# Performance work log

Hardware: AMD Instinct MI355X
Metric: run time of the kernel (lower is better)

Reference implementation:

```python
import jax, jax.numpy as jnp
import numpy as np

D_MODEL = 512
D_FF = 2048
VOCAB = 32000
B, N = 2, 384
EPS = 1e-6


def positional_encoding(n, d):
    pos = np.arange(n)[:, None].astype(np.float64)
    i = np.arange(d)[None, :]
    ang = pos / np.power(10000.0, (2 * (i // 2)) / np.float32(d))
    ang[:, 0::2] = np.sin(ang[:, 0::2])
    ang[:, 1::2] = np.cos(ang[:, 1::2])
    return jnp.asarray(ang, dtype=jnp.float32)  # [n, d]


def layer_norm(x, gamma, beta):
    mu = jnp.mean(x, axis=-1, keepdims=True)
    var = jnp.mean(jnp.square(x - mu), axis=-1, keepdims=True)
    return (x - mu) / jnp.sqrt(var + EPS) * gamma + beta


def setup_inputs() -> dict:
    key = jax.random.key(0)
    ks = jax.random.split(key, 12)
    s = 0.02
    return {
        "tokens": jax.random.randint(ks[0], (B, N), 0, VOCAB, dtype=jnp.int32),
        "emb": jax.random.normal(ks[1], (VOCAB, D_MODEL), jnp.float32) * s,
        "Wq": jax.random.normal(ks[2], (D_MODEL, D_MODEL), jnp.float32) * s,
        "bq": jnp.zeros((D_MODEL,), jnp.float32),
        "Wk": jax.random.normal(ks[3], (D_MODEL, D_MODEL), jnp.float32) * s,
        "bk": jnp.zeros((D_MODEL,), jnp.float32),
        "Wv": jax.random.normal(ks[4], (D_MODEL, D_MODEL), jnp.float32) * s,
        "bv": jnp.zeros((D_MODEL,), jnp.float32),
        "attn_scale": jax.random.normal(ks[5], (D_MODEL,), jnp.float32) * 0.05,
        "Wo": jax.random.normal(ks[6], (D_MODEL, D_MODEL), jnp.float32) * s,
        "bo": jnp.zeros((D_MODEL,), jnp.float32),
        "g1": jnp.ones((D_MODEL,), jnp.float32),
        "beta1": jnp.zeros((D_MODEL,), jnp.float32),
        "W1": jax.random.normal(ks[7], (D_MODEL, D_FF), jnp.float32) * s,
        "bf1": jnp.zeros((D_FF,), jnp.float32),
        "W2": jax.random.normal(ks[8], (D_FF, D_MODEL), jnp.float32) * s,
        "bf2": jnp.zeros((D_MODEL,), jnp.float32),
        "g2": jnp.ones((D_MODEL,), jnp.float32),
        "beta2": jnp.zeros((D_MODEL,), jnp.float32),
    }


def reference(tokens, emb, Wq, bq, Wk, bk, Wv, bv, attn_scale, Wo, bo,
              g1, beta1, W1, bf1, W2, bf2, g2, beta2):
    # Embedding + scaled positional encoding
    x = emb[tokens] * jnp.sqrt(jnp.float32(D_MODEL))  # [B, N, D]
    x = x + positional_encoding(N, D_MODEL)[None, :, :]

    # Additive (Bahdanau) self-attention
    q = x @ Wq + bq
    k = x @ Wk + bk  # note: original swaps key/value Dense layers; math-equivalent
    v = x @ Wv + bv
    # scores[b,i,j] = sum_d scale[d] * tanh(q[b,i,d] + k[b,j,d])  -> [B,N,N]
    scores = jnp.einsum("d,bijd->bij", attn_scale,
                        jnp.tanh(q[:, :, None, :] + k[:, None, :, :]))
    weights = jax.nn.softmax(scores, axis=-1)
    attn = jnp.einsum("bij,bjd->bid", weights, v)
    attn = attn @ Wo + bo
    x = layer_norm(x + attn, g1, beta1)

    # Feedforward + residual + LayerNorm
    h = jax.nn.relu(x @ W1 + bf1)
    y = h @ W2 + bf2
    return layer_norm(x + y, g2, beta2)
```

## Files before the change

kernel.cpp:

```cpp
#include <hip/hip_runtime.h>
#include <hip/hip_bf16.h>
#include <math.h>

#define D_MODEL 512
#define D_FF    2048
#define NBATCH  2
#define NSEQ    384
#define NROWS   (NBATCH * NSEQ)
#define LN_EPS  1e-6f

typedef __attribute__((ext_vector_type(8))) short short8;
typedef __attribute__((ext_vector_type(4))) short short4v;
typedef __attribute__((ext_vector_type(4))) float f32x4;
typedef __hip_bfloat16 bf16;

static __device__ __forceinline__ short bfb(float x) {
    bf16 h = __float2bfloat16(x);
    return *reinterpret_cast<short*>(&h);
}

#define MFMA16(a, b, c) __builtin_amdgcn_mfma_f32_16x16x32_bf16((a), (b), (c), 0, 0, 0)

__global__ __launch_bounds__(256) void prep_kernel(
    const int* __restrict__ tokens, const float* __restrict__ emb,
    const float* __restrict__ Wq, const float* __restrict__ Wk,
    const float* __restrict__ Wv, const float* __restrict__ Wo,
    const float* __restrict__ W1, const float* __restrict__ W2,
    bf16* __restrict__ wqt, bf16* __restrict__ wkt, bf16* __restrict__ wvt,
    bf16* __restrict__ wot, bf16* __restrict__ w1t, bf16* __restrict__ w2t,
    float* __restrict__ x, bf16* __restrict__ xb)
{
    __shared__ float tile[32][33];
    int t = blockIdx.x;

    if (t < 3072) {
        const float* W; bf16* Wt; int K, N, bx, by;
        if (t < 1024) {
            int w = t >> 8, rem = t & 255;
            W  = (w == 0) ? Wq  : (w == 1) ? Wk  : (w == 2) ? Wv  : Wo;
            Wt = (w == 0) ? wqt : (w == 1) ? wkt : (w == 2) ? wvt : wot;
            K = 512; N = 512; bx = rem & 15; by = rem >> 4;
        } else if (t < 2048) {
            int rem = t - 1024;
            W = W1; Wt = w1t; K = 512; N = 2048; bx = rem & 63; by = rem >> 6;
        } else {
            int rem = t - 2048;
            W = W2; Wt = w2t; K = 2048; N = 512; bx = rem & 15; by = rem >> 4;
        }
        int tx = threadIdx.x & 31, ty = threadIdx.x >> 5;
        #pragma unroll
        for (int r = ty; r < 32; r += 8)
            tile[r][tx] = W[(size_t)(by * 32 + r) * N + bx * 32 + tx];
        __syncthreads();
        #pragma unroll
        for (int r = ty; r < 32; r += 8)
            Wt[(size_t)(bx * 32 + r) * K + by * 32 + tx] = __float2bfloat16(tile[tx][r]);
    } else {
        int row = t - 3072;
        int n   = row % NSEQ;
        int tok = tokens[row];
        const float sqrtD = 22.627416997969522f;
        const float ESC   = 0.02595256324130752f;
        for (int d = threadIdx.x; d < D_MODEL; d += 256) {
            float e   = emb[tok * D_MODEL + d] * sqrtD;
            float ang = (float)n * __builtin_amdgcn_exp2f(-(float)(d & ~1) * ESC);
            float pe  = (d & 1) ? __cosf(ang) : __sinf(ang);
            float val = e + pe;
            x [(size_t)row * D_MODEL + d] = val;
            xb[(size_t)row * D_MODEL + d] = __float2bfloat16(val);
        }
    }
}

__global__ __launch_bounds__(256) void qkv_mfma_kernel(
    const bf16* __restrict__ A,
    const bf16* __restrict__ wqt, const bf16* __restrict__ wkt, const bf16* __restrict__ wvt,
    const float* __restrict__ bq, const float* __restrict__ bk, const float* __restrict__ bv,
    float* __restrict__ aexp, float* __restrict__ bexp, bf16* __restrict__ vT)
{
    int z = blockIdx.z;
    const bf16*  Wt   = (z == 0) ? wqt : (z == 1) ? wkt : wvt;
    const float* bias = (z == 0) ? bq  : (z == 1) ? bk  : bv;

    int lane = threadIdx.x & 63, wid = threadIdx.x >> 6;
    int rowBase = blockIdx.y * 32 + (wid >> 1) * 16;
    int colBase = blockIdx.x * 64 + (wid & 1) * 32;

    const bf16* Ap  = A  + (size_t)(rowBase + (lane & 15)) * D_MODEL + ((lane >> 4) << 3);
    const bf16* Bp0 = Wt + (size_t)(colBase + (lane & 15)) * D_MODEL + ((lane >> 4) << 3);
    const bf16* Bp1 = Bp0 + (size_t)16 * D_MODEL;

    f32x4 acc0 = {0.f, 0.f, 0.f, 0.f};
    f32x4 acc1 = {0.f, 0.f, 0.f, 0.f};

    #pragma unroll 4
    for (int k0 = 0; k0 < D_MODEL; k0 += 32) {
        short8 a  = *reinterpret_cast<const short8*>(Ap  + k0);
        short8 b0 = *reinterpret_cast<const short8*>(Bp0 + k0);
        short8 b1 = *reinterpret_cast<const short8*>(Bp1 + k0);
        acc0 = MFMA16(a, b0, acc0);
        acc1 = MFMA16(a, b1, acc1);
    }

    int crow = rowBase + ((lane >> 4) << 2);
    int ccol = colBase + (lane & 15);

    if (z < 2) {
        float* C = (z == 0) ? aexp : bexp;
        #pragma unroll
        for (int r = 0; r < 4; ++r) {
            int row = crow + r;
            #pragma unroll
            for (int j = 0; j < 2; ++j) {
                int col = ccol + j * 16;
                float val = (j == 0 ? acc0[r] : acc1[r]) + bias[col];
                C[(size_t)row * D_MODEL + col] = __expf(2.0f * val);
            }
        }
    } else {
        int bb = crow / NSEQ;
        int jr = crow - bb * NSEQ;
        #pragma unroll
        for (int j = 0; j < 2; ++j) {
            int col = ccol + j * 16;
            short4v pk;
            #pragma unroll
            for (int r = 0; r < 4; ++r)
                pk[r] = bfb((j == 0 ? acc0[r] : acc1[r]) + bias[col]);
            size_t idx = ((size_t)bb * D_MODEL + col) * NSEQ + jr;
            *reinterpret_cast<short4v*>((short*)vT + idx) = pk;
        }
    }
}

__global__ __launch_bounds__(512) void score_kernel(
    const float* __restrict__ aexp, const float* __restrict__ bexp,
    const float* __restrict__ scale, bf16* __restrict__ E,
    float* __restrict__ Sp)
{
    int ig   = blockIdx.x;
    int qt   = blockIdx.y;
    int row0 = ig * 4;
    int b    = row0 / NSEQ;
    int tid  = threadIdx.x;
    int lane = tid & 63, wid = tid >> 6;

    __shared__ float sred[8][4];

    const float* ap = aexp + (size_t)row0 * D_MODEL + lane * 8;
    float a[4][8];
    #pragma unroll
    for (int r = 0; r < 4; ++r) {
        float4 A0 = *(const float4*)(ap + (size_t)r * D_MODEL);
        float4 A1 = *(const float4*)(ap + (size_t)r * D_MODEL + 4);
        a[r][0]=A0.x; a[r][1]=A0.y; a[r][2]=A0.z; a[r][3]=A0.w;
        a[r][4]=A1.x; a[r][5]=A1.y; a[r][6]=A1.z; a[r][7]=A1.w;
    }
    float4 S0 = *(const float4*)(scale + lane * 8);
    float4 S1 = *(const float4*)(scale + lane * 8 + 4);
    float sv[8] = {-2.0f*S0.x,-2.0f*S0.y,-2.0f*S0.z,-2.0f*S0.w,
                   -2.0f*S1.x,-2.0f*S1.y,-2.0f*S1.z,-2.0f*S1.w};

    const float* kb = bexp + (size_t)b * NSEQ * D_MODEL + lane * 8;
    int jb = qt * 96 + wid;

    float es[4] = {0.f, 0.f, 0.f, 0.f};

    for (int t6 = 0; t6 < 6; ++t6) {
        int j0 = jb + t6 * 16;
        int j1 = j0 + 8;
        const float4* kp0 = (const float4*)(kb + (size_t)j0 * D_MODEL);
        const float4* kp1 = (const float4*)(kb + (size_t)j1 * D_MODEL);
        float4 xa = kp0[0], xc = kp0[1];
        float4 ya = kp1[0], yc = kp1[1];
        float b0[8] = {xa.x,xa.y,xa.z,xa.w,xc.x,xc.y,xc.z,xc.w};
        float b1[8] = {ya.x,ya.y,ya.z,ya.w,yc.x,yc.y,yc.z,yc.w};

        float u[4][2] = {};
        #pragma unroll
        for (int up = 0; up < 4; ++up) {
            int d0 = up * 2, d1 = d0 + 1;
            #pragma unroll
            for (int js = 0; js < 2; ++js) {
                float xx = js ? b1[d0] : b0[d0];
                float yy = js ? b1[d1] : b0[d1];
                #pragma unroll
                for (int r = 0; r < 4; ++r) {
                    float p   = fmaf(a[r][d0], xx, 1.0f);
                    float q   = fmaf(a[r][d1], yy, 1.0f);
                    float num = fmaf(sv[d0], q, sv[d1] * p);
                    u[r][js]  = fmaf(num, __builtin_amdgcn_rcpf(p * q), u[r][js]);
                }
            }
        }

        #pragma unroll
        for (int off = 1; off < 64; off <<= 1) {
            #pragma unroll
            for (int r = 0; r < 4; ++r) {
                u[r][0] += __shfl_xor(u[r][0], off, 64);
                u[r][1] += __shfl_xor(u[r][1], off, 64);
            }
        }

        #pragma unroll
        for (int r = 0; r < 4; ++r) {
            float e0 = __expf(u[r][0]);
            float e1 = __expf(u[r][1]);
            if (lane == 0) {
                E[(size_t)(row0 + r) * NSEQ + j0] = __float2bfloat16(e0);
                E[(size_t)(row0 + r) * NSEQ + j1] = __float2bfloat16(e1);
            }
            es[r] += e0 + e1;
        }
    }

    if (lane == 0) {
        sred[wid][0] = es[0]; sred[wid][1] = es[1];
        sred[wid][2] = es[2]; sred[wid][3] = es[3];
    }
    __syncthreads();
    if (tid < 4) {
        float s = 0.0f;
        #pragma unroll
        for (int w = 0; w < 8; ++w) s += sred[w][tid];
        Sp[(size_t)(row0 + tid) * 4 + qt] = s;
    }
}

__global__ __launch_bounds__(512) void pv_wo_ln_kernel(
    const bf16* __restrict__ E, const bf16* __restrict__ vT,
    const float* __restrict__ Sp, const bf16* __restrict__ wot,
    const float* __restrict__ bo, const float* __restrict__ x0,
    const float* __restrict__ g1, const float* __restrict__ beta1,
    float* __restrict__ x1, bf16* __restrict__ x1b)
{
    int row0 = blockIdx.x * 16;
    int b    = row0 / NSEQ;
    int tid  = threadIdx.x;
    int lane = tid & 63, wid = tid >> 6;
    int colBase = wid * 64;

    __shared__ bf16  attnS[16][D_MODEL + 8];
    __shared__ float t1f  [16][D_MODEL + 4];

    int arow = lane & 15;
    int koff = (lane >> 4) << 3;
    int crow = (lane >> 4) << 2;
    int ccol = lane & 15;

    {
        const bf16* Ap = E + ((size_t)(row0 + arow)) * NSEQ + koff;
        const bf16* Bp = vT + ((size_t)b * D_MODEL + colBase + arow) * NSEQ + koff;
        f32x4 p0 = {0,0,0,0}, p1 = {0,0,0,0}, p2 = {0,0,0,0}, p3 = {0,0,0,0};
        #pragma unroll
        for (int k0 = 0; k0 < NSEQ; k0 += 32) {
            short8 a  = *(const short8*)(Ap + k0);
            short8 v0 = *(const short8*)(Bp + k0);
            short8 v1 = *(const short8*)(Bp + (size_t)16 * NSEQ + k0);
            short8 v2 = *(const short8*)(Bp + (size_t)32 * NSEQ + k0);
            short8 v3 = *(const short8*)(Bp + (size_t)48 * NSEQ + k0);
            p0 = MFMA16(a, v0, p0);
            p1 = MFMA16(a, v1, p1);
            p2 = MFMA16(a, v2, p2);
            p3 = MFMA16(a, v3, p3);
        }
        #pragma unroll
        for (int r = 0; r < 4; ++r) {
            int lrow = crow + r;
            float4 sp4 = *(const float4*)(Sp + (size_t)(row0 + lrow) * 4);
            float Sinv = 1.0f / (sp4.x + sp4.y + sp4.z + sp4.w);
            attnS[lrow][colBase +  0 + ccol] = __float2bfloat16(p0[r] * Sinv);
            attnS[lrow][colBase + 16 + ccol] = __float2bfloat16(p1[r] * Sinv);
            attnS[lrow][colBase + 32 + ccol] = __float2bfloat16(p2[r] * Sinv);
            attnS[lrow][colBase + 48 + ccol] = __float2bfloat16(p3[r] * Sinv);
        }
    }
    __syncthreads();

    {
        const bf16* Wp = wot + ((size_t)(colBase + arow)) * D_MODEL + koff;
        f32x4 w0 = {0,0,0,0}, w1 = {0,0,0,0}, w2 = {0,0,0,0}, w3 = {0,0,0,0};
        #pragma unroll
        for (int k0 = 0; k0 < D_MODEL; k0 += 32) {
            short8 a  = *(const short8*)(&attnS[arow][k0 + koff]);
            short8 q0 = *(const short8*)(Wp + k0);
            short8 q1 = *(const short8*)(Wp + (size_t)16 * D_MODEL + k0);
            short8 q2 = *(const short8*)(Wp + (size_t)32 * D_MODEL + k0);
            short8 q3 = *(const short8*)(Wp + (size_t)48 * D_MODEL + k0);
            w0 = MFMA16(a, q0, w0);
            w1 = MFMA16(a, q1, w1);
            w2 = MFMA16(a, q2, w2);
            w3 = MFMA16(a, q3, w3);
        }
        #pragma unroll
        for (int r = 0; r < 4; ++r) {
            int lrow = crow + r;
            size_t grow = (size_t)(row0 + lrow);
            int c0 = colBase + ccol;
            t1f[lrow][c0     ] = w0[r] + bo[c0     ] + x0[grow * D_MODEL + c0     ];
            t1f[lrow][c0 + 16] = w1[r] + bo[c0 + 16] + x0[grow * D_MODEL + c0 + 16];
            t1f[lrow][c0 + 32] = w2[r] + bo[c0 + 32] + x0[grow * D_MODEL + c0 + 32];
            t1f[lrow][c0 + 48] = w3[r] + bo[c0 + 48] + x0[grow * D_MODEL + c0 + 48];
        }
    }
    __syncthreads();

    #pragma unroll
    for (int rr = 0; rr < 2; ++rr) {
        int lrow = wid * 2 + rr;
        size_t grow = (size_t)(row0 + lrow);
        float v[8];
        #pragma unroll
        for (int u = 0; u < 8; ++u) v[u] = t1f[lrow][lane * 8 + u];
        float s = 0.0f;
        #pragma unroll
        for (int u = 0; u < 8; ++u) s += v[u];
        #pragma unroll
        for (int off = 1; off < 64; off <<= 1) s += __shfl_xor(s, off, 64);
        float mu = s * (1.0f / D_MODEL);
        float s2 = 0.0f;
        #pragma unroll
        for (int u = 0; u < 8; ++u) { float d = v[u] - mu; s2 += d * d; }
        #pragma unroll
        for (int off = 1; off < 64; off <<= 1) s2 += __shfl_xor(s2, off, 64);
        float inv = rsqrtf(s2 * (1.0f / D_MODEL) + LN_EPS);
        #pragma unroll
        for (int u = 0; u < 8; ++u) {
            int c = lane * 8 + u;
            float o = (v[u] - mu) * inv * g1[c] + beta1[c];
            x1 [grow * D_MODEL + c] = o;
            x1b[grow * D_MODEL + c] = __float2bfloat16(o);
        }
    }
}

__global__ __launch_bounds__(256) void mfma_gemm_kernel(
    const bf16* __restrict__ A, const bf16* __restrict__ Wt,
    const float* __restrict__ bias,
    bf16* __restrict__ Cb, int K, int N, int relu)
{
    int lane = threadIdx.x & 63, wid = threadIdx.x >> 6;
    int rowBase = blockIdx.y * 32 + (wid >> 1) * 16;
    int colBase = blockIdx.x * 64 + (wid & 1) * 32;

    const bf16* Ap  = A  + (size_t)(rowBase + (lane & 15)) * K + ((lane >> 4) << 3);
    const bf16* Bp0 = Wt + (size_t)(colBase + (lane & 15)) * K + ((lane >> 4) << 3);
    const bf16* Bp1 = Bp0 + (size_t)16 * K;

    f32x4 acc0 = {0.f, 0.f, 0.f, 0.f};
    f32x4 acc1 = {0.f, 0.f, 0.f, 0.f};

    #pragma unroll 4
    for (int k0 = 0; k0 < K; k0 += 32) {
        short8 a  = *reinterpret_cast<const short8*>(Ap  + k0);
        short8 b0 = *reinterpret_cast<const short8*>(Bp0 + k0);
        short8 b1 = *reinterpret_cast<const short8*>(Bp1 + k0);
        acc0 = MFMA16(a, b0, acc0);
        acc1 = MFMA16(a, b1, acc1);
    }

    int crow = rowBase + ((lane >> 4) << 2);
    int ccol = colBase + (lane & 15);
    #pragma unroll
    for (int r = 0; r < 4; ++r) {
        int row = crow + r;
        #pragma unroll
        for (int j = 0; j < 2; ++j) {
            int col = ccol + j * 16;
            float val = (j == 0 ? acc0[r] : acc1[r]) + bias[col];
            if (relu) val = fmaxf(val, 0.0f);
            Cb[(size_t)row * N + col] = __float2bfloat16(val);
        }
    }
}

__global__ __launch_bounds__(256) void ffdown_kernel(
    const bf16* __restrict__ A, const bf16* __restrict__ Wt,
    const float* __restrict__ bias, const float* __restrict__ resid,
    float* __restrict__ y0, float* __restrict__ y1)
{
    int z = blockIdx.z;
    int kbeg = z * (D_FF / 2);
    int lane = threadIdx.x & 63, wid = threadIdx.x >> 6;
    int rowBase = blockIdx.y * 32 + (wid >> 1) * 16;
    int colBase = blockIdx.x * 64 + (wid & 1) * 32;

    const bf16* Ap  = A  + (size_t)(rowBase + (lane & 15)) * D_FF + kbeg + ((lane >> 4) << 3);
    const bf16* Bp0 = Wt + (size_t)(colBase + (lane & 15)) * D_FF + kbeg + ((lane >> 4) << 3);
    const bf16* Bp1 = Bp0 + (size_t)16 * D_FF;

    f32x4 acc0 = {0.f, 0.f, 0.f, 0.f};
    f32x4 acc1 = {0.f, 0.f, 0.f, 0.f};

    #pragma unroll 4
    for (int k0 = 0; k0 < D_FF / 2; k0 += 32) {
        short8 a  = *reinterpret_cast<const short8*>(Ap  + k0);
        short8 b0 = *reinterpret_cast<const short8*>(Bp0 + k0);
        short8 b1 = *reinterpret_cast<const short8*>(Bp1 + k0);
        acc0 = MFMA16(a, b0, acc0);
        acc1 = MFMA16(a, b1, acc1);
    }

    int crow = rowBase + ((lane >> 4) << 2);
    int ccol = colBase + (lane & 15);
    #pragma unroll
    for (int r = 0; r < 4; ++r) {
        int row = crow + r;
        #pragma unroll
        for (int j = 0; j < 2; ++j) {
            int col = ccol + j * 16;
            float val = (j == 0 ? acc0[r] : acc1[r]);
            if (z == 0) {
                val += bias[col] + resid[(size_t)row * D_MODEL + col];
                y0[(size_t)row * D_MODEL + col] = val;
            } else {
                y1[(size_t)row * D_MODEL + col] = val;
            }
        }
    }
}

__global__ __launch_bounds__(256) void ln_kernel(
    const float* __restrict__ in, const float* __restrict__ in2,
    const float* __restrict__ gamma, const float* __restrict__ beta,
    float* __restrict__ out)
{
    int row = blockIdx.x;
    int tid = threadIdx.x;
    int lane = tid & 63, wid = tid >> 6;
    __shared__ float red[4];

    float v0 = in[(size_t)row * D_MODEL + tid];
    float v1 = in[(size_t)row * D_MODEL + tid + 256];
    if (in2) {
        v0 += in2[(size_t)row * D_MODEL + tid];
        v1 += in2[(size_t)row * D_MODEL + tid + 256];
    }

    float s = v0 + v1;
    #pragma unroll
    for (int off = 32; off; off >>= 1) s += __shfl_xor(s, off, 64);
    if (lane == 0) red[wid] = s;
    __syncthreads();
    if (tid == 0) red[0] = red[0] + red[1] + red[2] + red[3];
    __syncthreads();
    float mu = red[0] * (1.0f / D_MODEL);
    __syncthreads();

    float d0 = v0 - mu, d1 = v1 - mu;
    float s2 = d0 * d0 + d1 * d1;
    #pragma unroll
    for (int off = 32; off; off >>= 1) s2 += __shfl_xor(s2, off, 64);
    if (lane == 0) red[wid] = s2;
    __syncthreads();
    if (tid == 0) red[0] = red[0] + red[1] + red[2] + red[3];
    __syncthreads();
    float var = red[0] * (1.0f / D_MODEL);
    float inv = rsqrtf(var + LN_EPS);

    out[(size_t)row * D_MODEL + tid]       = d0 * inv * gamma[tid] + beta[tid];
    out[(size_t)row * D_MODEL + tid + 256] = d1 * inv * gamma[tid + 256] + beta[tid + 256];
}

extern "C" void kernel_launch(void* const* d_in, const int* in_sizes, int n_in,
                              void* d_out, int out_size, void* d_ws, size_t ws_size,
                              hipStream_t stream)
{
    const int*   tokens = (const int*)  d_in[0];
    const float* emb    = (const float*)d_in[1];
    const float* Wq     = (const float*)d_in[2];
    const float* bq     = (const float*)d_in[3];
    const float* Wk     = (const float*)d_in[4];
    const float* bk     = (const float*)d_in[5];
    const float* Wv     = (const float*)d_in[6];
    const float* bv     = (const float*)d_in[7];
    const float* ascale = (const float*)d_in[8];
    const float* Wo     = (const float*)d_in[9];
    const float* bo     = (const float*)d_in[10];
    const float* g1     = (const float*)d_in[11];
    const float* beta1  = (const float*)d_in[12];
    const float* W1     = (const float*)d_in[13];
    const float* bf1    = (const float*)d_in[14];
    const float* W2     = (const float*)d_in[15];
    const float* bf2    = (const float*)d_in[16];
    const float* g2     = (const float*)d_in[17];
    const float* beta2  = (const float*)d_in[18];

    float* out = (float*)d_out;
    float* ws  = (float*)d_ws;

    const size_t SZ = (size_t)NROWS * D_MODEL;

    float* x0   = ws;
    float* aexp = ws + 1 * SZ;
    float* bexp = ws + 2 * SZ;
    float* x1 = aexp;
    float* y0 = x1;
    float* y1 = bexp;

    bf16* x0b   = (bf16*)(ws + 3 * SZ);
    bf16* x1b   = x0b + SZ;
    bf16* hb    = x1b + SZ;
    bf16* Eb    = hb + (size_t)NROWS * D_FF;
    bf16* vTb   = Eb + (size_t)NBATCH * NSEQ * NSEQ;
    bf16* wqt   = vTb + (size_t)NBATCH * D_MODEL * NSEQ;
    bf16* wkt   = wqt + (size_t)D_MODEL * D_MODEL;
    bf16* wvt   = wkt + (size_t)D_MODEL * D_MODEL;
    bf16* wot   = wvt + (size_t)D_MODEL * D_MODEL;
    bf16* w1t   = wot + (size_t)D_MODEL * D_MODEL;
    bf16* w2t   = w1t + (size_t)D_MODEL * D_FF;
    float* Sp   = (float*)(w2t + (size_t)D_FF * D_MODEL);

    prep_kernel<<<3072 + NROWS, 256, 0, stream>>>(
        tokens, emb, Wq, Wk, Wv, Wo, W1, W2,
        wqt, wkt, wvt, wot, w1t, w2t, x0, x0b);

    qkv_mfma_kernel<<<dim3(D_MODEL / 64, NROWS / 32, 3), 256, 0, stream>>>(
        x0b, wqt, wkt, wvt, bq, bk, bv, aexp, bexp, vTb);

    score_kernel<<<dim3(NROWS / 4, 4), 512, 0, stream>>>(aexp, bexp, ascale, Eb, Sp);

    pv_wo_ln_kernel<<<NROWS / 16, 512, 0, stream>>>(
        Eb, vTb, Sp, wot, bo, x0, g1, beta1, x1, x1b);

    mfma_gemm_kernel<<<dim3(D_FF / 64, NROWS / 32), 256, 0, stream>>>(
        x1b, w1t, bf1, hb, D_MODEL, D_FF, 1);

    ffdown_kernel<<<dim3(D_MODEL / 64, NROWS / 32, 2), 256, 0, stream>>>(
        hb, w2t, bf2, x1, y0, y1);

    ln_kernel<<<NROWS, 256, 0, stream>>>(y0, y1, g2, beta2, out);
}
```

Baseline: 134.2 us.

## Fuse PV product into score kernel and split Wo projection from LayerNorm

New measurement: 130.5 us. -2.7%, faster.

```diff
diff --git a/kernel.cpp b/kernel.cpp
--- a/kernel.cpp
+++ b/kernel.cpp
@@ -76,7 +76,7 @@
     const bf16* __restrict__ A,
     const bf16* __restrict__ wqt, const bf16* __restrict__ wkt, const bf16* __restrict__ wvt,
     const float* __restrict__ bq, const float* __restrict__ bk, const float* __restrict__ bv,
-    float* __restrict__ aexp, float* __restrict__ bexp, bf16* __restrict__ vT)
+    float* __restrict__ aexp, float* __restrict__ bexp, bf16* __restrict__ vb)
 {
     int z = blockIdx.z;
     const bf16*  Wt   = (z == 0) ? wqt : (z == 1) ? wkt : wvt;
@@ -118,25 +118,23 @@
             }
         }
     } else {
-        int bb = crow / NSEQ;
-        int jr = crow - bb * NSEQ;
-        #pragma unroll
-        for (int j = 0; j < 2; ++j) {
-            int col = ccol + j * 16;
-            short4v pk;
+        #pragma unroll
+        for (int r = 0; r < 4; ++r) {
+            int row = crow + r;
             #pragma unroll
-            for (int r = 0; r < 4; ++r)
-                pk[r] = bfb((j == 0 ? acc0[r] : acc1[r]) + bias[col]);
-            size_t idx = ((size_t)bb * D_MODEL + col) * NSEQ + jr;
-            *reinterpret_cast<short4v*>((short*)vT + idx) = pk;
-        }
-    }
-}
-
-__global__ __launch_bounds__(512) void score_kernel(
+            for (int j = 0; j < 2; ++j) {
+                int col = ccol + j * 16;
+                float val = (j == 0 ? acc0[r] : acc1[r]) + bias[col];
+                vb[(size_t)row * D_MODEL + col] = __float2bfloat16(val);
+            }
+        }
+    }
+}
+
+__global__ __launch_bounds__(512) void scorepv_kernel(
     const float* __restrict__ aexp, const float* __restrict__ bexp,
-    const float* __restrict__ scale, bf16* __restrict__ E,
-    float* __restrict__ Sp)
+    const float* __restrict__ scale, const bf16* __restrict__ vb,
+    float* __restrict__ attn_q, float* __restrict__ Sp)
 {
     int ig   = blockIdx.x;
     int qt   = blockIdx.y;
@@ -145,6 +143,7 @@
     int tid  = threadIdx.x;
     int lane = tid & 63, wid = tid >> 6;
 
+    __shared__ float Et[4][96];
     __shared__ float sred[8][4];
 
     const float* ap = aexp + (size_t)row0 * D_MODEL + lane * 8;
@@ -167,7 +166,9 @@
     float es[4] = {0.f, 0.f, 0.f, 0.f};
 
     for (int t6 = 0; t6 < 6; ++t6) {
-        int j0 = jb + t6 * 16;
+        int jl0 = wid + t6 * 16;
+        int jl1 = jl0 + 8;
+        int j0 = qt * 96 + jl0;
         int j1 = j0 + 8;
         const float4* kp0 = (const float4*)(kb + (size_t)j0 * D_MODEL);
         const float4* kp1 = (const float4*)(kb + (size_t)j1 * D_MODEL);
@@ -207,10 +208,7 @@
         for (int r = 0; r < 4; ++r) {
             float e0 = __expf(u[r][0]);
             float e1 = __expf(u[r][1]);
-            if (lane == 0) {
-                E[(size_t)(row0 + r) * NSEQ + j0] = __float2bfloat16(e0);
-                E[(size_t)(row0 + r) * NSEQ + j1] = __float2bfloat16(e1);
-            }
+            if (lane == 0) { Et[r][jl0] = e0; Et[r][jl1] = e1; }
             es[r] += e0 + e1;
         }
     }
@@ -226,111 +224,93 @@
         for (int w = 0; w < 8; ++w) s += sred[w][tid];
         Sp[(size_t)(row0 + tid) * 4 + qt] = s;
     }
-}
-
-__global__ __launch_bounds__(512) void pv_wo_ln_kernel(
-    const bf16* __restrict__ E, const bf16* __restrict__ vT,
-    const float* __restrict__ Sp, const bf16* __restrict__ wot,
-    const float* __restrict__ bo, const float* __restrict__ x0,
-    const float* __restrict__ g1, const float* __restrict__ beta1,
-    float* __restrict__ x1, bf16* __restrict__ x1b)
-{
-    int row0 = blockIdx.x * 16;
-    int b    = row0 / NSEQ;
-    int tid  = threadIdx.x;
+
+    int d = wid * 64 + lane;
+    const bf16* vcol = vb + ((size_t)b * NSEQ + qt * 96) * D_MODEL + d;
+    float pacc[4] = {0.f, 0.f, 0.f, 0.f};
+    #pragma unroll 4
+    for (int j = 0; j < 96; ++j) {
+        float vf = __bfloat162float(vcol[(size_t)j * D_MODEL]);
+        pacc[0] = fmaf(Et[0][j], vf, pacc[0]);
+        pacc[1] = fmaf(Et[1][j], vf, pacc[1]);
+        pacc[2] = fmaf(Et[2][j], vf, pacc[2]);
+        pacc[3] = fmaf(Et[3][j], vf, pacc[3]);
+    }
+    size_t qbase = (size_t)qt * NROWS * D_MODEL;
+    #pragma unroll
+    for (int r = 0; r < 4; ++r)
+        attn_q[qbase + (size_t)(row0 + r) * D_MODEL + d] = pacc[r];
+}
+
+__global__ __launch_bounds__(256) void wo_kernel(
+    const float* __restrict__ attn_q, const float* __restrict__ Sp,
+    const bf16* __restrict__ wot, const float* __restrict__ bo,
+    const float* __restrict__ x0, float* __restrict__ t1)
+{
+    int rowBase = blockIdx.y * 32;
+    int colBase = blockIdx.x * 64;
+    int tid = threadIdx.x;
+
+    __shared__ bf16  attnS[32][D_MODEL + 8];
+    __shared__ float sinvS[32];
+
+    if (tid < 32) {
+        float4 s4 = *(const float4*)(Sp + (size_t)(rowBase + tid) * 4);
+        sinvS[tid] = 1.0f / (s4.x + s4.y + s4.z + s4.w);
+    }
+    __syncthreads();
+
+    const size_t Q = (size_t)NROWS * D_MODEL;
+    #pragma unroll
+    for (int i = tid; i < 32 * D_MODEL / 4; i += 256) {
+        int r  = i >> 7;
+        int d4 = (i & 127) << 2;
+        size_t off = (size_t)(rowBase + r) * D_MODEL + d4;
+        float4 v0 = *(const float4*)(attn_q + off);
+        float4 v1 = *(const float4*)(attn_q + Q + off);
+        float4 v2 = *(const float4*)(attn_q + 2 * Q + off);
+        float4 v3 = *(const float4*)(attn_q + 3 * Q + off);
+        float si = sinvS[r];
+        short4v pk;
+        pk[0] = bfb((v0.x + v1.x + v2.x + v3.x) * si);
+        pk[1] = bfb((v0.y + v1.y + v2.y + v3.y) * si);
+        pk[2] = bfb((v0.z + v1.z + v2.z + v3.z) * si);
+        pk[3] = bfb((v0.w + v1.w + v2.w + v3.w) * si);
+        *reinterpret_cast<short4v*>(&attnS[r][d4]) = pk;
+    }
+    __syncthreads();
+
     int lane = tid & 63, wid = tid >> 6;
-    int colBase = wid * 64;
-
-    __shared__ bf16  attnS[16][D_MODEL + 8];
-    __shared__ float t1f  [16][D_MODEL + 4];
-
-    int arow = lane & 15;
-    int koff = (lane >> 4) << 3;
-    int crow = (lane >> 4) << 2;
-    int ccol = lane & 15;
-
-    {
-        const bf16* Ap = E + ((size_t)(row0 + arow)) * NSEQ + koff;
-        const bf16* Bp = vT + ((size_t)b * D_MODEL + colBase + arow) * NSEQ + koff;
-        f32x4 p0 = {0,0,0,0}, p1 = {0,0,0,0}, p2 = {0,0,0,0}, p3 = {0,0,0,0};
-        #pragma unroll
-        for (int k0 = 0; k0 < NSEQ; k0 += 32) {
-            short8 a  = *(const short8*)(Ap + k0);
-            short8 v0 = *(const short8*)(Bp + k0);
-            short8 v1 = *(const short8*)(Bp + (size_t)16 * NSEQ + k0);
-            short8 v2 = *(const short8*)(Bp + (size_t)32 * NSEQ + k0);
-            short8 v3 = *(const short8*)(Bp + (size_t)48 * NSEQ + k0);
-            p0 = MFMA16(a, v0, p0);
-            p1 = MFMA16(a, v1, p1);
-            p2 = MFMA16(a, v2, p2);
-            p3 = MFMA16(a, v3, p3);
-        }
-        #pragma unroll
-        for (int r = 0; r < 4; ++r) {
-            int lrow = crow + r;
-            float4 sp4 = *(const float4*)(Sp + (size_t)(row0 + lrow) * 4);
-            float Sinv = 1.0f / (sp4.x + sp4.y + sp4.z + sp4.w);
-            attnS[lrow][colBase +  0 + ccol] = __float2bfloat16(p0[r] * Sinv);
-            attnS[lrow][colBase + 16 + ccol] = __float2bfloat16(p1[r] * Sinv);
-            attnS[lrow][colBase + 32 + ccol] = __float2bfloat16(p2[r] * Sinv);
-            attnS[lrow][colBase + 48 + ccol] = __float2bfloat16(p3[r] * Sinv);
-        }
-    }
-    __syncthreads();
-
-    {
-        const bf16* Wp = wot + ((size_t)(colBase + arow)) * D_MODEL + koff;
-        f32x4 w0 = {0,0,0,0}, w1 = {0,0,0,0}, w2 = {0,0,0,0}, w3 = {0,0,0,0};
-        #pragma unroll
-        for (int k0 = 0; k0 < D_MODEL; k0 += 32) {
-            short8 a  = *(const short8*)(&attnS[arow][k0 + koff]);
-            short8 q0 = *(const short8*)(Wp + k0);
-            short8 q1 = *(const short8*)(Wp + (size_t)16 * D_MODEL + k0);
-            short8 q2 = *(const short8*)(Wp + (size_t)32 * D_MODEL + k0);
-            short8 q3 = *(const short8*)(Wp + (size_t)48 * D_MODEL + k0);
-            w0 = MFMA16(a, q0, w0);
-            w1 = MFMA16(a, q1, w1);
-            w2 = MFMA16(a, q2, w2);
-            w3 = MFMA16(a, q3, w3);
-        }
-        #pragma unroll
-        for (int r = 0; r < 4; ++r) {
-            int lrow = crow + r;
-            size_t grow = (size_t)(row0 + lrow);
-            int c0 = colBase + ccol;
-            t1f[lrow][c0     ] = w0[r] + bo[c0     ] + x0[grow * D_MODEL + c0     ];
-            t1f[lrow][c0 + 16] = w1[r] + bo[c0 + 16] + x0[grow * D_MODEL + c0 + 16];
-            t1f[lrow][c0 + 32] = w2[r] + bo[c0 + 32] + x0[grow * D_MODEL + c0 + 32];
-            t1f[lrow][c0 + 48] = w3[r] + bo[c0 + 48] + x0[grow * D_MODEL + c0 + 48];
-        }
-    }
-    __syncthreads();
-
-    #pragma unroll
-    for (int rr = 0; rr < 2; ++rr) {
-        int lrow = wid * 2 + rr;
-        size_t grow = (size_t)(row0 + lrow);
-        float v[8];
-        #pragma unroll
-        for (int u = 0; u < 8; ++u) v[u] = t1f[lrow][lane * 8 + u];
-        float s = 0.0f;
-        #pragma unroll
-        for (int u = 0; u < 8; ++u) s += v[u];
-        #pragma unroll
-        for (int off = 1; off < 64; off <<= 1) s += __shfl_xor(s, off, 64);
-        float mu = s * (1.0f / D_MODEL);
-        float s2 = 0.0f;
-        #pragma unroll
-        for (int u = 0; u < 8; ++u) { float d = v[u] - mu; s2 += d * d; }
-        #pragma unroll
-        for (int off = 1; off < 64; off <<= 1) s2 += __shfl_xor(s2, off, 64);
-        float inv = rsqrtf(s2 * (1.0f / D_MODEL) + LN_EPS);
-        #pragma unroll
-        for (int u = 0; u < 8; ++u) {
-            int c = lane * 8 + u;
-            float o = (v[u] - mu) * inv * g1[c] + beta1[c];
-            x1 [grow * D_MODEL + c] = o;
-            x1b[grow * D_MODEL + c] = __float2bfloat16(o);
+    int wrow = (wid >> 1) * 16;
+    int wcol = colBase + (wid & 1) * 32;
+    int arow = lane & 15, koff = (lane >> 4) << 3;
+
+    const bf16* Bp0 = wot + (size_t)(wcol + arow) * D_MODEL + koff;
+    const bf16* Bp1 = Bp0 + (size_t)16 * D_MODEL;
+
+    f32x4 acc0 = {0.f, 0.f, 0.f, 0.f};
+    f32x4 acc1 = {0.f, 0.f, 0.f, 0.f};
+
+    #pragma unroll 4
+    for (int k0 = 0; k0 < D_MODEL; k0 += 32) {
+        short8 a  = *reinterpret_cast<const short8*>(&attnS[wrow + arow][k0 + koff]);
+        short8 b0 = *reinterpret_cast<const short8*>(Bp0 + k0);
+        short8 b1 = *reinterpret_cast<const short8*>(Bp1 + k0);
+        acc0 = MFMA16(a, b0, acc0);
+        acc1 = MFMA16(a, b1, acc1);
+    }
+
+    int crow = rowBase + wrow + ((lane >> 4) << 2);
+    int ccol = wcol + (lane & 15);
+    #pragma unroll
+    for (int r = 0; r < 4; ++r) {
+        int row = crow + r;
+        #pragma unroll
+        for (int j = 0; j < 2; ++j) {
+            int col = ccol + j * 16;
+            float val = (j == 0 ? acc0[r] : acc1[r]) + bo[col]
+                      + x0[(size_t)row * D_MODEL + col];
+            t1[(size_t)row * D_MODEL + col] = val;
         }
     }
 }
@@ -424,7 +404,7 @@
 __global__ __launch_bounds__(256) void ln_kernel(
     const float* __restrict__ in, const float* __restrict__ in2,
     const float* __restrict__ gamma, const float* __restrict__ beta,
-    float* __restrict__ out)
+    float* __restrict__ out, bf16* __restrict__ outb)
 {
     int row = blockIdx.x;
     int tid = threadIdx.x;
@@ -459,8 +439,14 @@
     float var = red[0] * (1.0f / D_MODEL);
     float inv = rsqrtf(var + LN_EPS);
 
-    out[(size_t)row * D_MODEL + tid]       = d0 * inv * gamma[tid] + beta[tid];
-    out[(size_t)row * D_MODEL + tid + 256] = d1 * inv * gamma[tid + 256] + beta[tid + 256];
+    float o0 = d0 * inv * gamma[tid] + beta[tid];
+    float o1 = d1 * inv * gamma[tid + 256] + beta[tid + 256];
+    out[(size_t)row * D_MODEL + tid]       = o0;
+    out[(size_t)row * D_MODEL + tid + 256] = o1;
+    if (outb) {
+        outb[(size_t)row * D_MODEL + tid]       = __float2bfloat16(o0);
+        outb[(size_t)row * D_MODEL + tid + 256] = __float2bfloat16(o1);
+    }
 }
 
 extern "C" void kernel_launch(void* const* d_in, const int* in_sizes, int n_in,
@@ -492,19 +478,20 @@
 
     const size_t SZ = (size_t)NROWS * D_MODEL;
 
-    float* x0   = ws;
-    float* aexp = ws + 1 * SZ;
-    float* bexp = ws + 2 * SZ;
-    float* x1 = aexp;
+    float* x0     = ws;
+    float* aexp   = ws + 1 * SZ;
+    float* bexp   = ws + 2 * SZ;
+    float* attn_q = ws + 3 * SZ;
+    float* t1 = aexp;
+    float* x1 = bexp;
     float* y0 = x1;
-    float* y1 = bexp;
-
-    bf16* x0b   = (bf16*)(ws + 3 * SZ);
+    float* y1 = x0;
+
+    bf16* x0b   = (bf16*)(ws + 7 * SZ);
     bf16* x1b   = x0b + SZ;
     bf16* hb    = x1b + SZ;
-    bf16* Eb    = hb + (size_t)NROWS * D_FF;
-    bf16* vTb   = Eb + (size_t)NBATCH * NSEQ * NSEQ;
-    bf16* wqt   = vTb + (size_t)NBATCH * D_MODEL * NSEQ;
+    bf16* vbb   = hb + (size_t)NROWS * D_FF;
+    bf16* wqt   = vbb + SZ;
     bf16* wkt   = wqt + (size_t)D_MODEL * D_MODEL;
     bf16* wvt   = wkt + (size_t)D_MODEL * D_MODEL;
     bf16* wot   = wvt + (size_t)D_MODEL * D_MODEL;
@@ -517,12 +504,15 @@
         wqt, wkt, wvt, wot, w1t, w2t, x0, x0b);
 
     qkv_mfma_kernel<<<dim3(D_MODEL / 64, NROWS / 32, 3), 256, 0, stream>>>(
-        x0b, wqt, wkt, wvt, bq, bk, bv, aexp, bexp, vTb);
-
-    score_kernel<<<dim3(NROWS / 4, 4), 512, 0, stream>>>(aexp, bexp, ascale, Eb, Sp);
-
-    pv_wo_ln_kernel<<<NROWS / 16, 512, 0, stream>>>(
-        Eb, vTb, Sp, wot, bo, x0, g1, beta1, x1, x1b);
+        x0b, wqt, wkt, wvt, bq, bk, bv, aexp, bexp, vbb);
+
+    scorepv_kernel<<<dim3(NROWS / 4, 4), 512, 0, stream>>>(
+        aexp, bexp, ascale, vbb, attn_q, Sp);
+
+    wo_kernel<<<dim3(D_MODEL / 64, NROWS / 32), 256, 0, stream>>>(
+        attn_q, Sp, wot, bo, x0, t1);
+
+    ln_kernel<<<NROWS, 256, 0, stream>>>(t1, nullptr, g1, beta1, x1, x1b);
 
     mfma_gemm_kernel<<<dim3(D_FF / 64, NROWS / 32), 256, 0, stream>>>(
         x1b, w1t, bf1, hb, D_MODEL, D_FF, 1);
@@ -530,5 +520,5 @@
     ffdown_kernel<<<dim3(D_MODEL / 64, NROWS / 32, 2), 256, 0, stream>>>(
         hb, w2t, bf2, x1, y0, y1);
 
-    ln_kernel<<<NROWS, 256, 0, stream>>>(y0, y1, g2, beta2, out);
-}
+    ln_kernel<<<NROWS, 256, 0, stream>>>(y0, y1, g2, beta2, out, nullptr);
+}
```
